# Optimization experiments

Hardware: AMD Instinct MI355X
Metric: run time of the kernel (lower is better)

Reference implementation:

```python
import jax, jax.numpy as jnp
import numpy as np

B, N = 4, 2048
IN_F, OUT_F, H = 128, 128, 8
HD = OUT_F // H  # 16
ALPHA = 0.2       # LeakyReLU negative slope
TIME_DECAY = 0.1


def setup_inputs() -> dict:
    key = jax.random.key(0)
    k1, k2, k3, k4, k5 = jax.random.split(key, 5)
    node_features = jax.random.normal(k1, (B, N, IN_F), dtype=jnp.float32)
    adj_matrix = jax.random.randint(k2, (B, N, N), 0, 2, dtype=jnp.int32)
    time_matrix = jax.random.uniform(k3, (B, N, N), dtype=jnp.float32)
    # xavier_uniform with gain=1.414 as in the torch module
    def xavier(k, shape, fan_in, fan_out):
        bound = 1.414 * np.sqrt(6.0 / (fan_in + fan_out))
        return jax.random.uniform(k, shape, minval=-bound, maxval=bound, dtype=jnp.float32)
    W = xavier(k4, (H, IN_F, HD), IN_F, HD)
    a = xavier(k5, (H, 2 * HD, 1), 2 * HD, 1)
    return {"node_features": node_features, "adj_matrix": adj_matrix,
            "time_matrix": time_matrix, "W": W, "a": a}


def reference(node_features, adj_matrix, time_matrix, W, a):
    # time weights (eq 17): exp(-lambda * (t_max - t))
    current_time = jnp.max(time_matrix)
    time_weights = jnp.exp(-TIME_DECAY * (current_time - time_matrix))  # [B,N,N]

    # per-head projection: [B,H,N,HD]
    h = jnp.einsum('bni,hio->bhno', node_features, W)

    # decompose attention vector a = [a_src; a_dst] so we never build the
    # O(N^2 * 2*HD) concat tensor: e_ij = LeakyReLU(a_src.h_i + a_dst.h_j)
    a_src = a[:, :HD, 0]   # [H,HD]
    a_dst = a[:, HD:, 0]   # [H,HD]
    e_i = jnp.einsum('bhnd,hd->bhn', h, a_src)  # score contribution of node i
    e_j = jnp.einsum('bhnd,hd->bhn', h, a_dst)  # score contribution of node j
    e = e_i[:, :, :, None] + e_j[:, :, None, :]          # [B,H,N,N]
    e = jax.nn.leaky_relu(e, negative_slope=ALPHA)
    e = e * time_weights[:, None, :, :]

    # mask non-edges, normalize (dropout is identity in eval mode)
    mask = adj_matrix[:, None, :, :] == 0                 # [B,1->H,N,N]
    e = jnp.where(mask, -jnp.inf, e)
    attention = jax.nn.softmax(e, axis=-1)                # [B,H,N,N]

    # aggregate neighbors, merge heads, ELU
    out = jnp.einsum('bhij,bhjo->bhio', attention, h)     # [B,H,N,HD]
    out = jnp.transpose(out, (0, 2, 1, 3)).reshape(node_features.shape[0], node_features.shape[1], -1)
    return jax.nn.elu(out)
```

## Files before the change

### kernel.cpp

```cpp
#include <hip/hip_runtime.h>
#include <hip/hip_bf16.h>

#define BN    4
#define NN    2048
#define INF   128
#define HH    8
#define HD    16
#define ALPHA 0.2f
#define DECAY 0.1f

#define DLOG2E 0.14426950408889634f
#define LLOG2E 0.5287663729448977f

typedef __attribute__((ext_vector_type(8))) short short8;
typedef __attribute__((ext_vector_type(4))) float float4v;

__device__ __forceinline__ float bf2f(unsigned short u) {
    return __uint_as_float(((unsigned)u) << 16);
}

__launch_bounds__(256, 8)
__global__ void k_setup(const float* __restrict__ x,
                        const float* __restrict__ W,
                        const float* __restrict__ a,
                        const float* __restrict__ tm,
                        unsigned* __restrict__ ct,
                        __hip_bfloat16* __restrict__ h_t,
                        float* __restrict__ es, float* __restrict__ ed) {
    if (blockIdx.x < 1024) {
        const uint4* p = (const uint4*)tm;
        const int nvec = BN * NN * NN / 4;
        int idx = blockIdx.x * 256 + threadIdx.x;
        const int stride = 1024 * 256;
        unsigned m = 0u;
        for (int i = idx; i < nvec; i += stride) {
            uint4 v = p[i];
            m = max(m, v.x); m = max(m, v.y); m = max(m, v.z); m = max(m, v.w);
        }
        float fm = __uint_as_float(m);
        #pragma unroll
        for (int o = 32; o >= 1; o >>= 1) fm = fmaxf(fm, __shfl_xor(fm, o));
        __shared__ float sm[4];
        if ((threadIdx.x & 63) == 0) sm[threadIdx.x >> 6] = fm;
        __syncthreads();
        if (threadIdx.x == 0) {
            float mm = fmaxf(fmaxf(sm[0], sm[1]), fmaxf(sm[2], sm[3]));
            atomicMax(ct, __float_as_uint(mm));
        }
    } else {
        int bid = blockIdx.x - 1024;
        int sub = threadIdx.x >> 7;
        int tt  = threadIdx.x & 127;
        int nn  = bid * 2 + sub;
        __shared__ float xs[2][INF];
        xs[sub][tt] = x[(size_t)nn * INF + tt];
        __syncthreads();
        int h = tt >> 4, d = tt & 15;
        const float* Wp = W + (h * INF) * HD + d;
        float acc = 0.f;
        #pragma unroll 16
        for (int i = 0; i < INF; i++) acc += xs[sub][i] * Wp[i * HD];
        int b = nn >> 11, n = nn & 2047;
        h_t[((size_t)((b * HH + h) * HD + d)) * NN + n] = __float2bfloat16(acc);
        float s  = acc * a[h * 2 * HD + d];
        float dd = acc * a[h * 2 * HD + HD + d];
        #pragma unroll
        for (int o = 8; o >= 1; o >>= 1) { s += __shfl_xor(s, o); dd += __shfl_xor(dd, o); }
        if (d == 0) {
            es[(b * HH + h) * NN + n] = s;
            ed[(b * HH + h) * NN + n] = dd;
        }
    }
}

__launch_bounds__(512, 8)
__global__ void k_attn(const int* __restrict__ adj,
                       const float* __restrict__ tm,
                       const __hip_bfloat16* __restrict__ h_t,
                       const float* __restrict__ es, const float* __restrict__ ed,
                       const unsigned* __restrict__ ctp,
                       float* __restrict__ pacc, float* __restrict__ pl) {
    int t    = threadIdx.x;
    int w    = t >> 6;
    int lane = t & 63;
    int q    = lane >> 4;
    int im   = lane & 15;
    int bx   = blockIdx.x;
    int b    = bx >> 8;
    int half = (bx >> 7) & 1;
    int i0   = (bx & 127) << 4;
    int i    = i0 + im;
    int jb   = half << 10;
    const int R = 8;

    __shared__ float tws[2][16 * 128];

    float ctv = __uint_as_float(*ctp);
    float c0  = fmaf(-DLOG2E, ctv, LLOG2E);
    float es_i = es[(b * HH + w) * NN + i];

    const float* ed_p = ed + (size_t)(b * HH + w) * NN + jb + q * 8;
    const __hip_bfloat16* ht_p = h_t + ((size_t)((b * HH + w) * HD + im)) * NN + jb + q * 8;

    int srow = t >> 5;
    int sblk = t & 31;
    int soff = srow * 128 + ((sblk ^ (srow & 7)) << 2);
    const int*   adj_s = adj + ((size_t)(b * NN + i0 + srow)) * NN + jb + (sblk << 2);
    const float* tm_s  = tm  + ((size_t)(b * NN + i0 + srow)) * NN + jb + (sblk << 2);

    int rbase = im * 128;
    int rx    = im & 7;

    union { uint4 u; short8 v; } ones;
    ones.u = make_uint4(0x3F803F80u, 0x3F803F80u, 0x3F803F80u, 0x3F803F80u);

    float4v acc  = {0.f, 0.f, 0.f, 0.f};
    float4v accl = {0.f, 0.f, 0.f, 0.f};

    int4   pa = *(const int4*)(adj_s);
    float4 pt = *(const float4*)(tm_s);
    {
        float w0 = (pa.x != 0) ? exp2f(fmaf(DLOG2E, pt.x, c0)) : 0.f;
        float w1 = (pa.y != 0) ? exp2f(fmaf(DLOG2E, pt.y, c0)) : 0.f;
        float w2 = (pa.z != 0) ? exp2f(fmaf(DLOG2E, pt.z, c0)) : 0.f;
        float w3 = (pa.w != 0) ? exp2f(fmaf(DLOG2E, pt.w, c0)) : 0.f;
        *(float4*)&tws[0][soff] = make_float4(w0, w1, w2, w3);
    }
    pa = *(const int4*)(adj_s + 128);
    pt = *(const float4*)(tm_s + 128);
    __syncthreads();

    for (int r = 0; r < R; r++) {
        int cur = r & 1;
        if (r + 1 < R) {
            float w0 = (pa.x != 0) ? exp2f(fmaf(DLOG2E, pt.x, c0)) : 0.f;
            float w1 = (pa.y != 0) ? exp2f(fmaf(DLOG2E, pt.y, c0)) : 0.f;
            float w2 = (pa.z != 0) ? exp2f(fmaf(DLOG2E, pt.z, c0)) : 0.f;
            float w3 = (pa.w != 0) ? exp2f(fmaf(DLOG2E, pt.w, c0)) : 0.f;
            *(float4*)&tws[cur ^ 1][soff] = make_float4(w0, w1, w2, w3);
            if (r + 2 < R) {
                pa = *(const int4*)(adj_s + (r + 2) * 128);
                pt = *(const float4*)(tm_s + (r + 2) * 128);
            }
        }
        #pragma unroll
        for (int c4 = 0; c4 < 4; c4++) {
            int blk0 = c4 * 8 + 2 * q;
            float4 w01 = *(const float4*)&tws[cur][rbase + ((blk0 ^ rx) << 2)];
            float4 w23 = *(const float4*)&tws[cur][rbase + (((blk0 + 1) ^ rx) << 2)];
            int jglob = r * 128 + c4 * 32;
            float4 e0 = *(const float4*)(ed_p + jglob);
            float4 e1 = *(const float4*)(ed_p + jglob + 4);
            uint4  hv = *(const uint4*)(ht_p + jglob);

            float wv[8] = {w01.x, w01.y, w01.z, w01.w, w23.x, w23.y, w23.z, w23.w};
            float ev[8] = {e0.x, e0.y, e0.z, e0.w, e1.x, e1.y, e1.z, e1.w};

            unsigned u[8];
            #pragma unroll
            for (int k = 0; k < 8; k++) {
                float s0 = es_i + ev[k];
                float sc = fmaxf(s0, ALPHA * s0);
                float pv = exp2f(sc * wv[k]);
                unsigned b16 = __float_as_uint(pv) + 0x8000u;
                u[k] = (wv[k] > 0.f) ? b16 : 0u;
            }
            union { uint4 w; short8 v; } af;
            af.w.x = __builtin_amdgcn_perm(u[1], u[0], 0x07060302u);
            af.w.y = __builtin_amdgcn_perm(u[3], u[2], 0x07060302u);
            af.w.z = __builtin_amdgcn_perm(u[5], u[4], 0x07060302u);
            af.w.w = __builtin_amdgcn_perm(u[7], u[6], 0x07060302u);

            union { uint4 u; short8 v; } bf;
            bf.u = hv;
            acc  = __builtin_amdgcn_mfma_f32_16x16x32_bf16(af.v, bf.v, acc, 0, 0, 0);
            accl = __builtin_amdgcn_mfma_f32_16x16x32_bf16(af.v, ones.v, accl, 0, 0, 0);
        }
        __syncthreads();
    }

    float* pb = pacc + ((size_t)bx * 8 + w) * 256;
    #pragma unroll
    for (int r = 0; r < 4; r++) pb[(q * 4 + r) * 16 + im] = acc[r];
    if (im == 0) {
        #pragma unroll
        for (int r = 0; r < 4; r++) pl[(size_t)bx * 128 + w * 16 + q * 4 + r] = accl[r];
    }
}

__launch_bounds__(256, 8)
__global__ void k_fin(const float* __restrict__ pacc, const float* __restrict__ pl,
                      float* __restrict__ out) {
    int o = blockIdx.x * 256 + threadIdx.x;
    int b   = o >> 18;
    int rem = o & 262143;
    int i   = rem >> 7;
    int hd  = rem & 127;
    int h   = hd >> 4;
    int d   = hd & 15;
    int it  = i >> 4;
    int row = i & 15;
    int blk0 = (b * 2 + 0) * 128 + it;
    int blk1 = blk0 + 128;
    float a0 = pacc[((size_t)blk0 * 8 + h) * 256 + row * 16 + d];
    float a1 = pacc[((size_t)blk1 * 8 + h) * 256 + row * 16 + d];
    float l  = pl[(size_t)blk0 * 128 + h * 16 + row]
             + pl[(size_t)blk1 * 128 + h * 16 + row];
    float v = (a0 + a1) / l;
    v = (v > 0.f) ? v : expm1f(v);
    out[o] = v;
}

extern "C" void kernel_launch(void* const* d_in, const int* in_sizes, int n_in,
                              void* d_out, int out_size, void* d_ws, size_t ws_size,
                              hipStream_t stream) {
    const float* x   = (const float*)d_in[0];
    const int*   adj = (const int*)d_in[1];
    const float* tm  = (const float*)d_in[2];
    const float* W   = (const float*)d_in[3];
    const float* a   = (const float*)d_in[4];
    float* out = (float*)d_out;

    float* wsf = (float*)d_ws;
    unsigned* ct = (unsigned*)wsf;
    float* es = wsf + 64;
    float* ed = es + BN * HH * NN;
    __hip_bfloat16* h_t = (__hip_bfloat16*)(ed + BN * HH * NN);
    float* pacc = (float*)(h_t + BN * HH * HD * NN);
    float* pl   = pacc + 1024 * 2048;

    hipMemsetAsync(d_ws, 0, 4, stream);
    k_setup<<<1024 + 4096, 256, 0, stream>>>(x, W, a, tm, ct, h_t, es, ed);
    k_attn <<<BN * 2 * (NN / 16), 512, 0, stream>>>(adj, tm, h_t, es, ed, ct, pacc, pl);
    k_fin  <<<(BN * NN * HH * HD) / 256, 256, 0, stream>>>(pacc, pl, out);
}
```

Baseline: 246.6 us.

## Drop column split in attention kernel and fuse finalize into its epilogue

Each attention block now walks all 2048 columns (R doubled) instead of half. Because the block holds the full row, it normalizes, applies ELU and writes the output directly, so the partial-sum buffers and the separate finalize kernel go away. This saves one launch and the partial write/read traffic, but halves the grid to 512 blocks, which may underfill the GPU. Launch bounds occupancy hint is also lowered from 8 to 4.

```diff
diff --git a/kernel.cpp b/kernel.cpp
--- a/kernel.cpp
+++ b/kernel.cpp
@@ -14,10 +14,6 @@
 
 typedef __attribute__((ext_vector_type(8))) short short8;
 typedef __attribute__((ext_vector_type(4))) float float4v;
-
-__device__ __forceinline__ float bf2f(unsigned short u) {
-    return __uint_as_float(((unsigned)u) << 16);
-}
 
 __launch_bounds__(256, 8)
 __global__ void k_setup(const float* __restrict__ x,
@@ -73,25 +69,23 @@
     }
 }
 
-__launch_bounds__(512, 8)
+__launch_bounds__(512, 4)
 __global__ void k_attn(const int* __restrict__ adj,
                        const float* __restrict__ tm,
                        const __hip_bfloat16* __restrict__ h_t,
                        const float* __restrict__ es, const float* __restrict__ ed,
                        const unsigned* __restrict__ ctp,
-                       float* __restrict__ pacc, float* __restrict__ pl) {
+                       float* __restrict__ out) {
     int t    = threadIdx.x;
     int w    = t >> 6;
     int lane = t & 63;
     int q    = lane >> 4;
     int im   = lane & 15;
     int bx   = blockIdx.x;
-    int b    = bx >> 8;
-    int half = (bx >> 7) & 1;
+    int b    = bx >> 7;
     int i0   = (bx & 127) << 4;
     int i    = i0 + im;
-    int jb   = half << 10;
-    const int R = 8;
+    const int R = 16;
 
     __shared__ float tws[2][16 * 128];
 
@@ -99,14 +93,14 @@
     float c0  = fmaf(-DLOG2E, ctv, LLOG2E);
     float es_i = es[(b * HH + w) * NN + i];
 
-    const float* ed_p = ed + (size_t)(b * HH + w) * NN + jb + q * 8;
-    const __hip_bfloat16* ht_p = h_t + ((size_t)((b * HH + w) * HD + im)) * NN + jb + q * 8;
+    const float* ed_p = ed + (size_t)(b * HH + w) * NN + q * 8;
+    const __hip_bfloat16* ht_p = h_t + ((size_t)((b * HH + w) * HD + im)) * NN + q * 8;
 
     int srow = t >> 5;
     int sblk = t & 31;
     int soff = srow * 128 + ((sblk ^ (srow & 7)) << 2);
-    const int*   adj_s = adj + ((size_t)(b * NN + i0 + srow)) * NN + jb + (sblk << 2);
-    const float* tm_s  = tm  + ((size_t)(b * NN + i0 + srow)) * NN + jb + (sblk << 2);
+    const int*   adj_s = adj + ((size_t)(b * NN + i0 + srow)) * NN + (sblk << 2);
+    const float* tm_s  = tm  + ((size_t)(b * NN + i0 + srow)) * NN + (sblk << 2);
 
     int rbase = im * 128;
     int rx    = im & 7;
@@ -179,36 +173,13 @@
         __syncthreads();
     }
 
-    float* pb = pacc + ((size_t)bx * 8 + w) * 256;
     #pragma unroll
-    for (int r = 0; r < 4; r++) pb[(q * 4 + r) * 16 + im] = acc[r];
-    if (im == 0) {
-        #pragma unroll
-        for (int r = 0; r < 4; r++) pl[(size_t)bx * 128 + w * 16 + q * 4 + r] = accl[r];
-    }
-}
-
-__launch_bounds__(256, 8)
-__global__ void k_fin(const float* __restrict__ pacc, const float* __restrict__ pl,
-                      float* __restrict__ out) {
-    int o = blockIdx.x * 256 + threadIdx.x;
-    int b   = o >> 18;
-    int rem = o & 262143;
-    int i   = rem >> 7;
-    int hd  = rem & 127;
-    int h   = hd >> 4;
-    int d   = hd & 15;
-    int it  = i >> 4;
-    int row = i & 15;
-    int blk0 = (b * 2 + 0) * 128 + it;
-    int blk1 = blk0 + 128;
-    float a0 = pacc[((size_t)blk0 * 8 + h) * 256 + row * 16 + d];
-    float a1 = pacc[((size_t)blk1 * 8 + h) * 256 + row * 16 + d];
-    float l  = pl[(size_t)blk0 * 128 + h * 16 + row]
-             + pl[(size_t)blk1 * 128 + h * 16 + row];
-    float v = (a0 + a1) / l;
-    v = (v > 0.f) ? v : expm1f(v);
-    out[o] = v;
+    for (int r = 0; r < 4; r++) {
+        int row = q * 4 + r;
+        float v = acc[r] / accl[r];
+        v = (v > 0.f) ? v : expm1f(v);
+        out[((size_t)(b * NN + i0 + row)) * (HH * HD) + w * HD + im] = v;
+    }
 }
 
 extern "C" void kernel_launch(void* const* d_in, const int* in_sizes, int n_in,
@@ -226,11 +197,8 @@
     float* es = wsf + 64;
     float* ed = es + BN * HH * NN;
     __hip_bfloat16* h_t = (__hip_bfloat16*)(ed + BN * HH * NN);
-    float* pacc = (float*)(h_t + BN * HH * HD * NN);
-    float* pl   = pacc + 1024 * 2048;
 
     hipMemsetAsync(d_ws, 0, 4, stream);
     k_setup<<<1024 + 4096, 256, 0, stream>>>(x, W, a, tm, ct, h_t, es, ed);
-    k_attn <<<BN * 2 * (NN / 16), 512, 0, stream>>>(adj, tm, h_t, es, ed, ct, pacc, pl);
-    k_fin  <<<(BN * NN * HH * HD) / 256, 256, 0, stream>>>(pacc, pl, out);
+    k_attn <<<BN * (NN / 16), 512, 0, stream>>>(adj, tm, h_t, es, ed, ct, out);
 }
```

Result: faster. 235.7 us (-4.4%).
